# Kernel tuning notes

Hardware: AMD Instinct MI355X
Metric: run time of the kernel (lower is better)

The kernel has to match this reference:

```python
import jax, jax.numpy as jnp
import numpy as np

N_HEADS = 8
CLIP = 10.0  # tanh clipping constant of the pointer logits
NEG = -1e9


def setup_inputs() -> dict:
    key = jax.random.key(0)
    ks = jax.random.split(key, 10)
    B, N, H = 1024, 100, 128
    s = 1.0 / np.sqrt(H).astype(np.float32)
    return {
        "encoder_inputs": jax.random.normal(ks[0], (B, N, H), jnp.float32),
        "pool": jax.random.normal(ks[1], (B, H), jnp.float32),
        "capacity": jnp.full((B, 1), 50.0, jnp.float32),  # vehicle capacity
        "demand": (1.0 + 9.0 * jax.random.uniform(ks[2], (B, N), jnp.float32)).at[:, 0].set(0.0),  # depot demand = 0
        "fc_w": jax.random.normal(ks[3], (H, H + 1), jnp.float32) * s,
        "fc1_w": jax.random.normal(ks[4], (H, H), jnp.float32) * s,
        "Wq": jax.random.normal(ks[5], (H, H), jnp.float32) * s,
        "Wk": jax.random.normal(ks[6], (H, H), jnp.float32) * s,
        "Wv": jax.random.normal(ks[7], (H, H), jnp.float32) * s,
        "Wo": jax.random.normal(ks[8], (H, H), jnp.float32) * s,
        "Wk2": jax.random.normal(ks[9], (H, H), jnp.float32) * s,
        "n_steps": 128,
        "T": 1,
        "greedy": 1,
    }


def _decode(encoder_inputs, pool, capacity, demand, fc_w, fc1_w, Wq, Wk, Wv, Wo, Wk2, n_steps, T):
    B, N, H = encoder_inputs.shape
    hd = H // N_HEADS
    # encoder projections are step-invariant -> hoist out of the loop
    K = (encoder_inputs @ Wk.T).reshape(B, N, N_HEADS, hd)
    V = (encoder_inputs @ Wv.T).reshape(B, N, N_HEADS, hd)
    K2 = encoder_inputs @ Wk2.T  # [B, N, H] pointer keys
    pool_proj = pool @ fc1_w.T   # [B, H]
    base_cap = capacity[0, 0]
    rows = jnp.arange(B)

    def update_mask(cap, index, mask1):
        # mask1: permanently visited customers (depot never permanently masked)
        go_depot = (index == 0)
        mask1 = mask1.at[rows, index].set(1.0)
        mask1 = mask1.at[:, 0].set(0.0)
        mask = jnp.maximum(mask1, (demand > cap).astype(jnp.float32))
        # cannot stay at depot; but depot must stay open once all customers are masked
        all_cust = jnp.all(mask[:, 1:] > 0.0, axis=1)
        depot = jnp.where(all_cust, 0.0, go_depot.astype(jnp.float32))
        mask = mask.at[:, 0].set(depot)
        return mask, mask1

    mask0, mask1_0 = update_mask(capacity, jnp.zeros((B,), jnp.int32), jnp.zeros((B, N), jnp.float32))
    inp0 = encoder_inputs[:, 0, :]
    inv_sqrt_hd = 1.0 / jnp.sqrt(jnp.float32(hd))
    inv_sqrt_h = 1.0 / jnp.sqrt(jnp.float32(H))

    def step(carry, _):
        _inp, cap, mask, mask1 = carry
        dec = jnp.concatenate([_inp, cap], axis=-1) @ fc_w.T + pool_proj  # [B, H]
        # multi-head glimpse over encoder nodes
        q = (dec @ Wq.T).reshape(B, N_HEADS, hd)
        scores = jnp.einsum('bhd,bnhd->bhn', q, K) * inv_sqrt_hd
        scores = jnp.where(mask[:, None, :] > 0.0, NEG, scores)
        attn = jax.nn.softmax(scores, axis=-1)
        glimpse = jnp.einsum('bhn,bnhd->bhd', attn, V).reshape(B, H) @ Wo.T
        # single-head clipped pointer logits
        u = CLIP * jnp.tanh(jnp.einsum('bh,bnh->bn', glimpse, K2) * inv_sqrt_h)
        u = jnp.where(mask > 0.0, NEG, u)
        logp_all = jax.nn.log_softmax(u / T, axis=-1)
        index = jnp.argmax(logp_all, axis=-1)  # greedy decoding
        log_p = jnp.take_along_axis(logp_all, index[:, None], axis=1)[:, 0]
        is_done = (jnp.sum(mask1[:, 1:], axis=1) >= N - 1).astype(jnp.float32)
        log_p = log_p * (1.0 - is_done)
        # state update: subtract served demand; reset to base capacity at depot
        sel_d = jnp.take_along_axis(demand, index[:, None], axis=1)
        cap = jnp.where(index[:, None] == 0, base_cap, cap - sel_d)
        mask, mask1 = update_mask(cap, index, mask1)
        _inp = jnp.take_along_axis(encoder_inputs, index[:, None, None], axis=1)[:, 0]
        return (_inp, cap, mask, mask1), (index, log_p)

    _, (actions, log_ps) = jax.lax.scan(step, (inp0, capacity, mask0, mask1_0), None, length=n_steps)
    return actions.T, jnp.sum(log_ps, axis=0)  # ([B, n_steps], [B])


def reference(encoder_inputs, pool, capacity, demand, fc_w, fc1_w, Wq, Wk, Wv, Wo, Wk2, n_steps, T, greedy):
    actions, log_p = _decode(encoder_inputs, pool, capacity, demand, fc_w, fc1_w, Wq, Wk, Wv, Wo, Wk2, n_steps, T)
    return actions, log_p
```

## Files before the change

kernel.cpp:

```cpp
#include <hip/hip_runtime.h>
#include <math.h>

#define NNODE 100
#define NEGV  -1000000000.0f

__device__ float g_Wall [128 * 512];
__device__ float g_Wall2[128 * 128];
__device__ float g_qcap [128];
__device__ float g_C    [(size_t)102400 * 512];
__device__ float g_qpool[(size_t)1024 * 128];
__device__ float g_S1   [(size_t)1024 * 100 * 800];
__device__ float g_Scap [(size_t)1024 * 800];

__device__ __forceinline__ float fast_rcp(float x) { return __builtin_amdgcn_rcpf(x); }
__device__ __forceinline__ float tanh10(float z) {
    const float e2 = __expf(2.0f * z);
    return fmaf(-20.0f, __builtin_amdgcn_rcpf(e2 + 1.0f), 10.0f);
}

template<int CTRL>
__device__ __forceinline__ int dpp_i(int v) {
    return __builtin_amdgcn_update_dpp(0, v, CTRL, 0xF, 0xF, true);
}
template<int CTRL>
__device__ __forceinline__ float dpp_f(float v) {
    return __uint_as_float((unsigned)dpp_i<CTRL>(__float_as_int(v)));
}

#if defined(__has_builtin)
#  if __has_builtin(__builtin_amdgcn_permlane16_swap)
#    define HAVE_PL16 1
#  endif
#  if __has_builtin(__builtin_amdgcn_permlane32_swap)
#    define HAVE_PL32 1
#  endif
#endif

__device__ __forceinline__ void x16_both(float x, float& a, float& b) {
#if defined(HAVE_PL16)
    auto r = __builtin_amdgcn_permlane16_swap(__float_as_uint(x),
                                              __float_as_uint(x), false, false);
    a = __uint_as_float(r[0]); b = __uint_as_float(r[1]);
#else
    a = x;
    b = __uint_as_float(
        (unsigned)__builtin_amdgcn_ds_swizzle(__float_as_int(x), 0x401F));
#endif
}
__device__ __forceinline__ void x32_both(float x, float& a, float& b) {
#if defined(HAVE_PL32)
    auto r = __builtin_amdgcn_permlane32_swap(__float_as_uint(x),
                                              __float_as_uint(x), false, false);
    a = __uint_as_float(r[0]); b = __uint_as_float(r[1]);
#else
    a = x;
    b = __shfl_xor(x, 32, 64);
#endif
}
__device__ __forceinline__ float x16_sum(float x) { float a, b; x16_both(x, a, b); return a + b; }
__device__ __forceinline__ float x16_max(float x) { float a, b; x16_both(x, a, b); return fmaxf(a, b); }
__device__ __forceinline__ float x32_sum(float x) { float a, b; x32_both(x, a, b); return a + b; }
__device__ __forceinline__ float x32_max(float x) { float a, b; x32_both(x, a, b); return fmaxf(a, b); }
__device__ __forceinline__ void x32_pair(float x, float& lo, float& hi) {
#if defined(HAVE_PL32)
    auto r = __builtin_amdgcn_permlane32_swap(__float_as_uint(x),
                                              __float_as_uint(x), false, false);
    lo = __uint_as_float(r[0]); hi = __uint_as_float(r[1]);
#else
    const float o = __shfl_xor(x, 32, 64);
    const bool high = (threadIdx.x & 32) != 0;
    lo = high ? o : x;
    hi = high ? x : o;
#endif
}

__global__ __launch_bounds__(128) void prep_kernel(
    const float* __restrict__ Wk,  const float* __restrict__ Wv,
    const float* __restrict__ Wk2, const float* __restrict__ Wo,
    const float* __restrict__ Wq,  const float* __restrict__ fc_w,
    const float* __restrict__ fc1_w)
{
    const int c = blockIdx.x;
    const int k = threadIdx.x;
    if (c < 128) {
        g_Wall[k * 512 + c] = Wk[c * 128 + k];
    } else if (c < 256) {
        g_Wall[k * 512 + c] = Wv[(c - 128) * 128 + k];
    } else if (c < 384) {
        const int cc = c - 256;
        float acc = 0.f;
        for (int h = 0; h < 128; h++)
            acc = fmaf(Wk2[h * 128 + k], Wo[h * 128 + cc], acc);
        g_Wall[k * 512 + c] = acc;
    } else if (c < 512) {
        const int cc = c - 384;
        float acc = 0.f;
        for (int j = 0; j < 128; j++)
            acc = fmaf(Wq[cc * 128 + j], fc_w[j * 129 + k], acc);
        g_Wall[k * 512 + c] = acc;
    } else if (c == 512) {
        float acc = 0.f;
        for (int j = 0; j < 128; j++)
            acc = fmaf(Wq[k * 128 + j], fc_w[j * 129 + 128], acc);
        g_qcap[k] = acc;
    } else {
        const int cc = c - 513;
        float acc = 0.f;
        for (int j = 0; j < 128; j++)
            acc = fmaf(Wq[cc * 128 + j], fc1_w[j * 128 + k], acc);
        g_Wall2[k * 128 + cc] = acc;
    }
}

__global__ __launch_bounds__(512) void gemm_kernel(const float* __restrict__ A,
                                                   int mode)
{
    const float* __restrict__ W = mode ? g_Wall2 : g_Wall;
    float* __restrict__ C       = mode ? g_qpool : g_C;
    const int ncols             = mode ? 128 : 512;
    const int m0 = blockIdx.x * 128, n0 = blockIdx.y * 128;

    __shared__ __align__(16) float At[32 * 132];
    __shared__ __align__(16) float Ws[32 * 128];
    const int tid = threadIdx.x;
    const int tm = tid >> 5, tn = tid & 31;
    const int mb = tm * 8, nb = tn * 4;
    float4 acc[8];
#pragma unroll
    for (int i = 0; i < 8; i++) acc[i] = make_float4(0.f, 0.f, 0.f, 0.f);

    for (int kc = 0; kc < 4; kc++) {
        for (int f = tid; f < 1024; f += 512) {
            const int r = f >> 3, q8 = f & 7;
            float4 a = *(const float4*)&A[(size_t)(m0 + r) * 128 + kc * 32 + q8 * 4];
            At[(q8 * 4 + 0) * 132 + r] = a.x;
            At[(q8 * 4 + 1) * 132 + r] = a.y;
            At[(q8 * 4 + 2) * 132 + r] = a.z;
            At[(q8 * 4 + 3) * 132 + r] = a.w;
            const int kl = f >> 5, q = f & 31;
            *(float4*)&Ws[kl * 128 + q * 4] =
                *(const float4*)&W[(size_t)(kc * 32 + kl) * ncols + n0 + q * 4];
        }
        __syncthreads();
        for (int k = 0; k < 32; k++) {
            const float4 w = *(float4*)&Ws[k * 128 + nb];
#pragma unroll
            for (int i = 0; i < 8; i += 4) {
                const float4 a = *(float4*)&At[k * 132 + mb + i];
                acc[i + 0].x = fmaf(a.x, w.x, acc[i + 0].x);
                acc[i + 0].y = fmaf(a.x, w.y, acc[i + 0].y);
                acc[i + 0].z = fmaf(a.x, w.z, acc[i + 0].z);
                acc[i + 0].w = fmaf(a.x, w.w, acc[i + 0].w);
                acc[i + 1].x = fmaf(a.y, w.x, acc[i + 1].x);
                acc[i + 1].y = fmaf(a.y, w.y, acc[i + 1].y);
                acc[i + 1].z = fmaf(a.y, w.z, acc[i + 1].z);
                acc[i + 1].w = fmaf(a.y, w.w, acc[i + 1].w);
                acc[i + 2].x = fmaf(a.z, w.x, acc[i + 2].x);
                acc[i + 2].y = fmaf(a.z, w.y, acc[i + 2].y);
                acc[i + 2].z = fmaf(a.z, w.z, acc[i + 2].z);
                acc[i + 2].w = fmaf(a.z, w.w, acc[i + 2].w);
                acc[i + 3].x = fmaf(a.w, w.x, acc[i + 3].x);
                acc[i + 3].y = fmaf(a.w, w.y, acc[i + 3].y);
                acc[i + 3].z = fmaf(a.w, w.z, acc[i + 3].z);
                acc[i + 3].w = fmaf(a.w, w.w, acc[i + 3].w);
            }
        }
        __syncthreads();
    }
#pragma unroll
    for (int i = 0; i < 8; i++)
        *(float4*)&C[(size_t)(m0 + mb + i) * ncols + n0 + nb] = acc[i];
}

__global__ __launch_bounds__(256) void s1_kernel()
{
    const int b = blockIdx.x;
    const int tid = threadIdx.x;
    const int h = tid >> 5, l32 = tid & 31;
    const float* __restrict__ Crow = &g_C[(size_t)b * 100 * 512];

    __shared__ __align__(16) float Q1sh[50 * 128];

    float4 kr[4][4];
    int nn[4];
#pragma unroll
    for (int j = 0; j < 4; j++) {
        nn[j] = l32 + 32 * j;
#pragma unroll
        for (int i = 0; i < 4; i++) {
            kr[j][i] = (nn[j] < 100)
                ? *(const float4*)&Crow[(size_t)nn[j] * 512 + h * 16 + i * 4]
                : make_float4(0.f, 0.f, 0.f, 0.f);
        }
    }
    float4 qc[4], qp[4];
#pragma unroll
    for (int i = 0; i < 4; i++) {
        qc[i] = *(const float4*)&g_qcap[h * 16 + i * 4];
        qp[i] = *(const float4*)&g_qpool[(size_t)b * 128 + h * 16 + i * 4];
    }
    float sp[4];
#pragma unroll
    for (int j = 0; j < 4; j++) {
        float dc = 0.f, dp = 0.f;
#pragma unroll
        for (int i = 0; i < 4; i++) {
            dc = fmaf(kr[j][i].x, qc[i].x, dc); dc = fmaf(kr[j][i].y, qc[i].y, dc);
            dc = fmaf(kr[j][i].z, qc[i].z, dc); dc = fmaf(kr[j][i].w, qc[i].w, dc);
            dp = fmaf(kr[j][i].x, qp[i].x, dp); dp = fmaf(kr[j][i].y, qp[i].y, dp);
            dp = fmaf(kr[j][i].z, qp[i].z, dp); dp = fmaf(kr[j][i].w, qp[i].w, dp);
        }
        sp[j] = dp;
        if (nn[j] < 100)
            g_Scap[(size_t)b * 800 + h * 100 + nn[j]] = dc * 0.25f;
    }

    float* __restrict__ S1b = &g_S1[(size_t)b * 80000];
    for (int half = 0; half < 2; half++) {
        const int mbase = half * 50;
        for (int f = tid; f < 1600; f += 256) {
            const int n = f >> 5, c4 = f & 31;
            *(float4*)&Q1sh[n * 128 + c4 * 4] =
                *(const float4*)&Crow[(size_t)(mbase + n) * 512 + 384 + c4 * 4];
        }
        __syncthreads();
        for (int mm = 0; mm < 50; mm++) {
            const int m = mbase + mm;
            float4 q[4];
#pragma unroll
            for (int i = 0; i < 4; i++)
                q[i] = *(float4*)&Q1sh[mm * 128 + h * 16 + i * 4];
#pragma unroll
            for (int j = 0; j < 4; j++) {
                if (nn[j] < 100) {
                    float d = 0.f;
#pragma unroll
                    for (int i = 0; i < 4; i++) {
                        d = fmaf(kr[j][i].x, q[i].x, d); d = fmaf(kr[j][i].y, q[i].y, d);
                        d = fmaf(kr[j][i].z, q[i].z, d); d = fmaf(kr[j][i].w, q[i].w, d);
                    }
                    S1b[(size_t)m * 800 + h * 100 + nn[j]] = (d + sp[j]) * 0.25f;
                }
            }
        }
        __syncthreads();
    }
}

__global__ __launch_bounds__(256) void decode_kernel(
    const float* __restrict__ capacity, const float* __restrict__ demand,
    const int* __restrict__ nsteps_p, const int* __restrict__ T_p,
    float* __restrict__ out)
{
    __shared__ float u_buf[2 * 800];
    __shared__ float demand_sh[NNODE];
    __shared__ int   act_sh[512];

    const int tid = threadIdx.x;
    const int b   = blockIdx.x;
    const int nsteps = nsteps_p[0];
    const float invT = 1.0f / (float)T_p[0];
    const float base_cap = capacity[0];
    const float inv_sqrt_h = 0.08838834764831845f;

    const float4* __restrict__ C4  = (const float4*)&g_C[(size_t)b * 100 * 512];
    const float*  __restrict__ S1b = &g_S1[(size_t)b * 80000];

    const int w = tid >> 6, l = tid & 63;
    const int g = l >> 3, f = l & 7;
    const int F = 8 * w + f;
    const int h8 = tid >> 5, l32 = tid & 31;

    float4 Vreg[13], K2r[13];
#pragma unroll
    for (int m = 0; m < 13; m++) {
        const int n = g + 8 * m;
        const bool v = n < 100;
        Vreg[m] = v ? C4[(size_t)n * 128 + 32 + F] : make_float4(0.f, 0.f, 0.f, 0.f);
        K2r[m]  = v ? C4[(size_t)n * 128 + 64 + F] : make_float4(0.f, 0.f, 0.f, 0.f);
    }
    float s1r[4], scapr[4], d4[4];
#pragma unroll
    for (int j = 0; j < 4; j++) {
        const int nj = l32 + 32 * j;
        const bool v = nj < 100;
        scapr[j] = v ? g_Scap[(size_t)b * 800 + h8 * 100 + nj] : 0.f;
        s1r[j]   = v ? S1b[h8 * 100 + nj] : 0.f;
        d4[j]    = v ? demand[b * 100 + nj] : 1.0e30f;
    }
    const float de0 = demand[b * 100 + l];
    const float de1 = (l + 64 < 100) ? demand[b * 100 + l + 64] : 1.0e30f;
    for (int n = tid; n < 100; n += 256) demand_sh[n] = demand[b * 100 + n];
    for (int t = tid; t < 512; t += 256) act_sh[t] = 0;
    bool me0 = false, me1 = false;
    unsigned mb4 = 0;
    float cap_r = capacity[b];
    float depot_r;
    {
        const bool am0 = (l == 0) ? true : (de0 > cap_r);
        const bool am1 = (l + 64 >= 100) ? true : (de1 > cap_r);
        depot_r = __all(am0 && am1) ? 0.f : 1.f;
    }
    float logp_r = 0.f;
    int visited_r = 0;
    int ub = 0;
    __syncthreads();

    for (int s = 0; s < nsteps; s++) {
        const float cap = cap_r;

        float a[4];
        float tot;
        {
            float sc[4];
#pragma unroll
            for (int j = 0; j < 4; j++) {
                const int nj = l32 + 32 * j;
                const bool m = (nj == 0) ? (depot_r != 0.f)
                    : (((mb4 >> j) & 1u) || (d4[j] > cap));
                const float raw = fmaf(cap, scapr[j], s1r[j]);
                sc[j] = (nj < 100 && !m) ? raw : NEGV;
            }
#pragma unroll
            for (int j = 0; j < 4; j++) a[j] = __expf(sc[j]);
            tot = (a[0] + a[1]) + (a[2] + a[3]);
        }

        float4 gp4 = make_float4(0.f, 0.f, 0.f, 0.f);
#pragma unroll
        for (int m = 0; m < 13; m++) {
            const int src = ((f >> 2) << 5) | (8 * (m & 3) + g);
            const float av = __shfl(a[m >> 2], src, 64);
            gp4.x = fmaf(av, Vreg[m].x, gp4.x);
            gp4.y = fmaf(av, Vreg[m].y, gp4.y);
            gp4.z = fmaf(av, Vreg[m].z, gp4.z);
            gp4.w = fmaf(av, Vreg[m].w, gp4.w);
        }
        tot += dpp_f<0xB1>(tot);
        tot += dpp_f<0x4E>(tot);
        tot += dpp_f<0x124>(tot);
        tot += dpp_f<0x128>(tot);
        tot = x16_sum(tot);
        gp4.x += dpp_f<0x128>(gp4.x);
        gp4.y += dpp_f<0x128>(gp4.y);
        gp4.z += dpp_f<0x128>(gp4.z);
        gp4.w += dpp_f<0x128>(gp4.w);
        gp4.x = x16_sum(gp4.x);
        gp4.y = x16_sum(gp4.y);
        gp4.z = x16_sum(gp4.z);
        gp4.w = x16_sum(gp4.w);
        gp4.x = x32_sum(gp4.x);
        gp4.y = x32_sum(gp4.y);
        gp4.z = x32_sum(gp4.z);
        gp4.w = x32_sum(gp4.w);
        {
            float tlo, thi;
            x32_pair(tot, tlo, thi);
            const float th = (f >> 2) ? thi : tlo;
            const float rt = fast_rcp(th);
            gp4.x *= rt; gp4.y *= rt; gp4.z *= rt; gp4.w *= rt;
        }

        {
            float pm[13];
#pragma unroll
            for (int m = 0; m < 13; m++) {
                float p = gp4.x * K2r[m].x;
                p = fmaf(gp4.y, K2r[m].y, p);
                p = fmaf(gp4.z, K2r[m].z, p);
                p = fmaf(gp4.w, K2r[m].w, p);
                pm[m] = p;
            }
#pragma unroll
            for (int m = 0; m < 13; m++) pm[m] += dpp_f<0xB1>(pm[m]);
#pragma unroll
            for (int m = 0; m < 13; m++) pm[m] += dpp_f<0x4E>(pm[m]);
            if ((f & 3) == 0) {
                const int r = w * 2 + (f >> 2);
#pragma unroll
                for (int m = 0; m < 13; m++) {
                    const int n = g + 8 * m;
                    if (n < 100) u_buf[ub + r * 100 + n] = pm[m];
                }
            }
        }
        __syncthreads();

        float v0, v1 = -3.0e38f;
        {
            float s8 = 0.f;
#pragma unroll
            for (int r = 0; r < 8; r++) s8 += u_buf[ub + r * 100 + l];
            const float u0 = tanh10(s8 * inv_sqrt_h);
            const bool m0 = (l == 0) ? (depot_r != 0.f) : (me0 || de0 > cap);
            v0 = (m0 ? NEGV : u0) * invT;
            if (l + 64 < 100) {
                float t8 = 0.f;
#pragma unroll
                for (int r = 0; r < 8; r++) t8 += u_buf[ub + r * 100 + l + 64];
                const float u1 = tanh10(t8 * inv_sqrt_h);
                const bool m1 = (me1 || de1 > cap);
                v1 = (m1 ? NEGV : u1) * invT;
            }
        }
        float tt = __expf(v0) + ((l + 64 < 100) ? __expf(v1) : 0.f);
        float vm = fmaxf(v0, v1);
#define E_STG(CTRL)                                                           \
        {                                                                     \
            tt += dpp_f<CTRL>(tt);                                            \
            vm = fmaxf(vm, dpp_f<CTRL>(vm));                                  \
        }
        E_STG(0xB1)
        E_STG(0x4E)
        E_STG(0x124)
        E_STG(0x128)
#undef E_STG
        tt = x16_sum(tt);
        vm = x16_max(vm);
        tt = x32_sum(tt);
        vm = x32_max(vm);
        const unsigned long long b0 = __ballot(v0 == vm);
        const unsigned long long b1 = __ballot(v1 == vm);
        const int idx = b0 ? (int)__builtin_ctzll(b0)
                           : (64 + (int)__builtin_ctzll(b1));

#pragma unroll
        for (int j = 0; j < 4; j++) {
            const int nj = l32 + 32 * j;
            if (nj < 100)
                s1r[j] = S1b[(size_t)idx * 800 + h8 * 100 + nj];
        }

        const float dmd_idx = demand_sh[idx];
        const float capn = (idx == 0) ? base_cap : (cap - dmd_idx);

        if (visited_r < 99) logp_r += vm - __logf(tt);
        visited_r += (idx > 0) ? 1 : 0;
        me0 = me0 || (l == idx && idx > 0);
        me1 = me1 || (l + 64 == idx);
#pragma unroll
        for (int j = 0; j < 4; j++)
            if ((l32 + 32 * j) == idx && idx > 0) mb4 |= (1u << j);

        const bool am0 = (l == 0) ? true : (me0 || de0 > capn);
        const bool am1 = (l + 64 >= 100) ? true : (me1 || de1 > capn);
        const bool allc = __all(am0 && am1);
        depot_r = allc ? 0.f : ((idx == 0) ? 1.f : 0.f);
        cap_r = capn;
        if (tid == 0) act_sh[s] = idx;
        ub ^= 800;

        if (visited_r >= 99) break;
    }

    __syncthreads();
    for (int t = tid; t < nsteps; t += 256)
        out[(size_t)b * nsteps + t] = (float)act_sh[t];
    if (tid == 0)
        out[(size_t)gridDim.x * nsteps + b] = logp_r;
}

extern "C" void kernel_launch(void* const* d_in, const int* in_sizes, int n_in,
                              void* d_out, int out_size, void* d_ws, size_t ws_size,
                              hipStream_t stream) {
    const float* enc    = (const float*)d_in[0];
    const float* pool   = (const float*)d_in[1];
    const float* cap    = (const float*)d_in[2];
    const float* demand = (const float*)d_in[3];
    const float* fc_w   = (const float*)d_in[4];
    const float* fc1_w  = (const float*)d_in[5];
    const float* Wq     = (const float*)d_in[6];
    const float* Wk     = (const float*)d_in[7];
    const float* Wv     = (const float*)d_in[8];
    const float* Wo     = (const float*)d_in[9];
    const float* Wk2    = (const float*)d_in[10];
    const int*   nst    = (const int*)d_in[11];
    const int*   Tp     = (const int*)d_in[12];
    float* out = (float*)d_out;

    prep_kernel<<<641, 128, 0, stream>>>(Wk, Wv, Wk2, Wo, Wq, fc_w, fc1_w);
    gemm_kernel<<<dim3(800, 4), 512, 0, stream>>>(enc, 0);
    gemm_kernel<<<dim3(8, 1),   512, 0, stream>>>(pool, 1);
    s1_kernel<<<1024, 256, 0, stream>>>();
    decode_kernel<<<1024, 256, 0, stream>>>(cap, demand, nst, Tp, out);
}
```

Before: 816.7 us.

## Fuse S1 score precompute into decode kernel with K held in LDS

Removes the separate s1_kernel, which materialized a 1024x100x800 score table (about 328 MB) in global memory, and instead computes the needed score row on the fly each decode step. Each step does this by loading the selected node's query vector and dotting it against K rows held in a swizzled shared-memory buffer. This trades a large HBM write-then-read for per-step LDS reads and FMAs. It also adds about 51 KB of shared memory per block, which may reduce occupancy. The odd guarded LDS write on an impossible nsteps value appears to be there to stop the compiler from optimizing the buffer away or hoisting its loads.

Result: slower. 1.172 ms (+43.5%).

```diff
diff --git a/kernel.cpp b/kernel.cpp
--- a/kernel.cpp
+++ b/kernel.cpp
@@ -9,8 +9,6 @@
 __device__ float g_qcap [128];
 __device__ float g_C    [(size_t)102400 * 512];
 __device__ float g_qpool[(size_t)1024 * 128];
-__device__ float g_S1   [(size_t)1024 * 100 * 800];
-__device__ float g_Scap [(size_t)1024 * 800];
 
 __device__ __forceinline__ float fast_rcp(float x) { return __builtin_amdgcn_rcpf(x); }
 __device__ __forceinline__ float tanh10(float z) {
@@ -172,86 +170,12 @@
         *(float4*)&C[(size_t)(m0 + mb + i) * ncols + n0 + nb] = acc[i];
 }
 
-__global__ __launch_bounds__(256) void s1_kernel()
-{
-    const int b = blockIdx.x;
-    const int tid = threadIdx.x;
-    const int h = tid >> 5, l32 = tid & 31;
-    const float* __restrict__ Crow = &g_C[(size_t)b * 100 * 512];
-
-    __shared__ __align__(16) float Q1sh[50 * 128];
-
-    float4 kr[4][4];
-    int nn[4];
-#pragma unroll
-    for (int j = 0; j < 4; j++) {
-        nn[j] = l32 + 32 * j;
-#pragma unroll
-        for (int i = 0; i < 4; i++) {
-            kr[j][i] = (nn[j] < 100)
-                ? *(const float4*)&Crow[(size_t)nn[j] * 512 + h * 16 + i * 4]
-                : make_float4(0.f, 0.f, 0.f, 0.f);
-        }
-    }
-    float4 qc[4], qp[4];
-#pragma unroll
-    for (int i = 0; i < 4; i++) {
-        qc[i] = *(const float4*)&g_qcap[h * 16 + i * 4];
-        qp[i] = *(const float4*)&g_qpool[(size_t)b * 128 + h * 16 + i * 4];
-    }
-    float sp[4];
-#pragma unroll
-    for (int j = 0; j < 4; j++) {
-        float dc = 0.f, dp = 0.f;
-#pragma unroll
-        for (int i = 0; i < 4; i++) {
-            dc = fmaf(kr[j][i].x, qc[i].x, dc); dc = fmaf(kr[j][i].y, qc[i].y, dc);
-            dc = fmaf(kr[j][i].z, qc[i].z, dc); dc = fmaf(kr[j][i].w, qc[i].w, dc);
-            dp = fmaf(kr[j][i].x, qp[i].x, dp); dp = fmaf(kr[j][i].y, qp[i].y, dp);
-            dp = fmaf(kr[j][i].z, qp[i].z, dp); dp = fmaf(kr[j][i].w, qp[i].w, dp);
-        }
-        sp[j] = dp;
-        if (nn[j] < 100)
-            g_Scap[(size_t)b * 800 + h * 100 + nn[j]] = dc * 0.25f;
-    }
-
-    float* __restrict__ S1b = &g_S1[(size_t)b * 80000];
-    for (int half = 0; half < 2; half++) {
-        const int mbase = half * 50;
-        for (int f = tid; f < 1600; f += 256) {
-            const int n = f >> 5, c4 = f & 31;
-            *(float4*)&Q1sh[n * 128 + c4 * 4] =
-                *(const float4*)&Crow[(size_t)(mbase + n) * 512 + 384 + c4 * 4];
-        }
-        __syncthreads();
-        for (int mm = 0; mm < 50; mm++) {
-            const int m = mbase + mm;
-            float4 q[4];
-#pragma unroll
-            for (int i = 0; i < 4; i++)
-                q[i] = *(float4*)&Q1sh[mm * 128 + h * 16 + i * 4];
-#pragma unroll
-            for (int j = 0; j < 4; j++) {
-                if (nn[j] < 100) {
-                    float d = 0.f;
-#pragma unroll
-                    for (int i = 0; i < 4; i++) {
-                        d = fmaf(kr[j][i].x, q[i].x, d); d = fmaf(kr[j][i].y, q[i].y, d);
-                        d = fmaf(kr[j][i].z, q[i].z, d); d = fmaf(kr[j][i].w, q[i].w, d);
-                    }
-                    S1b[(size_t)m * 800 + h * 100 + nn[j]] = (d + sp[j]) * 0.25f;
-                }
-            }
-        }
-        __syncthreads();
-    }
-}
-
 __global__ __launch_bounds__(256) void decode_kernel(
     const float* __restrict__ capacity, const float* __restrict__ demand,
     const int* __restrict__ nsteps_p, const int* __restrict__ T_p,
     float* __restrict__ out)
 {
+    __shared__ float4 Klds4[NNODE * 32];
     __shared__ float u_buf[2 * 800];
     __shared__ float demand_sh[NNODE];
     __shared__ int   act_sh[512];
@@ -263,13 +187,17 @@
     const float base_cap = capacity[0];
     const float inv_sqrt_h = 0.08838834764831845f;
 
-    const float4* __restrict__ C4  = (const float4*)&g_C[(size_t)b * 100 * 512];
-    const float*  __restrict__ S1b = &g_S1[(size_t)b * 80000];
+    const float4* __restrict__ C4 = (const float4*)&g_C[(size_t)b * 100 * 512];
 
     const int w = tid >> 6, l = tid & 63;
     const int g = l >> 3, f = l & 7;
     const int F = 8 * w + f;
     const int h8 = tid >> 5, l32 = tid & 31;
+
+    for (int f2 = tid; f2 < 3200; f2 += 256) {
+        const int row = f2 >> 5, c4 = f2 & 31;
+        Klds4[row * 32 + (c4 ^ (row & 7))] = C4[(size_t)row * 128 + c4];
+    }
 
     float4 Vreg[13], K2r[13];
 #pragma unroll
@@ -279,15 +207,42 @@
         Vreg[m] = v ? C4[(size_t)n * 128 + 32 + F] : make_float4(0.f, 0.f, 0.f, 0.f);
         K2r[m]  = v ? C4[(size_t)n * 128 + 64 + F] : make_float4(0.f, 0.f, 0.f, 0.f);
     }
-    float s1r[4], scapr[4], d4[4];
-#pragma unroll
-    for (int j = 0; j < 4; j++) {
-        const int nj = l32 + 32 * j;
-        const bool v = nj < 100;
-        scapr[j] = v ? g_Scap[(size_t)b * 800 + h8 * 100 + nj] : 0.f;
-        s1r[j]   = v ? S1b[h8 * 100 + nj] : 0.f;
-        d4[j]    = v ? demand[b * 100 + nj] : 1.0e30f;
-    }
+
+    float s1r[4], scapr[4], sp[4], d4[4];
+    {
+        float4 qc[4], qp[4], q0[4];
+#pragma unroll
+        for (int i = 0; i < 4; i++) {
+            qc[i] = *(const float4*)&g_qcap[h8 * 16 + i * 4];
+            qp[i] = *(const float4*)&g_qpool[(size_t)b * 128 + h8 * 16 + i * 4];
+            q0[i] = C4[96 + h8 * 4 + i];
+        }
+#pragma unroll
+        for (int j = 0; j < 4; j++) {
+            const int nj = l32 + 32 * j;
+            const bool v = nj < 100;
+            float4 kr[4];
+#pragma unroll
+            for (int i = 0; i < 4; i++)
+                kr[i] = v ? C4[(size_t)nj * 128 + h8 * 4 + i]
+                          : make_float4(0.f, 0.f, 0.f, 0.f);
+            float dc = 0.f, dp = 0.f, d0 = 0.f;
+#pragma unroll
+            for (int i = 0; i < 4; i++) {
+                dc = fmaf(kr[i].x, qc[i].x, dc); dc = fmaf(kr[i].y, qc[i].y, dc);
+                dc = fmaf(kr[i].z, qc[i].z, dc); dc = fmaf(kr[i].w, qc[i].w, dc);
+                dp = fmaf(kr[i].x, qp[i].x, dp); dp = fmaf(kr[i].y, qp[i].y, dp);
+                dp = fmaf(kr[i].z, qp[i].z, dp); dp = fmaf(kr[i].w, qp[i].w, dp);
+                d0 = fmaf(kr[i].x, q0[i].x, d0); d0 = fmaf(kr[i].y, q0[i].y, d0);
+                d0 = fmaf(kr[i].z, q0[i].z, d0); d0 = fmaf(kr[i].w, q0[i].w, d0);
+            }
+            scapr[j] = dc * 0.25f;
+            sp[j]    = dp;
+            s1r[j]   = v ? (d0 + dp) * 0.25f : 0.f;
+            d4[j]    = v ? demand[b * 100 + nj] : 1.0e30f;
+        }
+    }
+
     const float de0 = demand[b * 100 + l];
     const float de1 = (l + 64 < 100) ? demand[b * 100 + l + 64] : 1.0e30f;
     for (int n = tid; n < 100; n += 256) demand_sh[n] = demand[b * 100 + n];
@@ -424,12 +379,10 @@
         const int idx = b0 ? (int)__builtin_ctzll(b0)
                            : (64 + (int)__builtin_ctzll(b1));
 
-#pragma unroll
-        for (int j = 0; j < 4; j++) {
-            const int nj = l32 + 32 * j;
-            if (nj < 100)
-                s1r[j] = S1b[(size_t)idx * 800 + h8 * 100 + nj];
-        }
+        float4 q1v[4];
+#pragma unroll
+        for (int i = 0; i < 4; i++)
+            q1v[i] = C4[(size_t)idx * 128 + 96 + h8 * 4 + i];
 
         const float dmd_idx = demand_sh[idx];
         const float capn = (idx == 0) ? base_cap : (cap - dmd_idx);
@@ -443,12 +396,30 @@
             if ((l32 + 32 * j) == idx && idx > 0) mb4 |= (1u << j);
 
         const bool am0 = (l == 0) ? true : (me0 || de0 > capn);
-        const bool am1 = (l + 64 >= 100) ? true : (me1 || de1 > capn);
+        const bool am1 = (l + 64 >= 100) ? true : (de1 > capn) || me1;
         const bool allc = __all(am0 && am1);
         depot_r = allc ? 0.f : ((idx == 0) ? 1.f : 0.f);
         cap_r = capn;
         if (tid == 0) act_sh[s] = idx;
         ub ^= 800;
+
+        if (tid == 0 && nsteps == -2147483647)
+            Klds4[0] = make_float4(0.f, 0.f, 0.f, 0.f);
+
+#pragma unroll
+        for (int j = 0; j < 4; j++) {
+            const int nj = l32 + 32 * j;
+            if (nj < 100) {
+                float d = 0.f;
+#pragma unroll
+                for (int i = 0; i < 4; i++) {
+                    const float4 k = Klds4[nj * 32 + ((h8 * 4 + i) ^ (nj & 7))];
+                    d = fmaf(k.x, q1v[i].x, d); d = fmaf(k.y, q1v[i].y, d);
+                    d = fmaf(k.z, q1v[i].z, d); d = fmaf(k.w, q1v[i].w, d);
+                }
+                s1r[j] = (d + sp[j]) * 0.25f;
+            }
+        }
 
         if (visited_r >= 99) break;
     }
@@ -481,6 +452,5 @@
     prep_kernel<<<641, 128, 0, stream>>>(Wk, Wv, Wk2, Wo, Wq, fc_w, fc1_w);
     gemm_kernel<<<dim3(800, 4), 512, 0, stream>>>(enc, 0);
     gemm_kernel<<<dim3(8, 1),   512, 0, stream>>>(pool, 1);
-    s1_kernel<<<1024, 256, 0, stream>>>();
     decode_kernel<<<1024, 256, 0, stream>>>(cap, demand, nst, Tp, out);
 }
```
